# Kernel optimization log

Measured on AMD Instinct MI355X. Metric: run time of the kernel, lower is better.

The kernel has to match this reference:

```python
import jax, jax.numpy as jnp
import numpy as np

B, S, E, H = 4, 2048, 1024, 16
D = E // H  # head_dim


def setup_inputs() -> dict:
    key = jax.random.key(0)
    ks = jax.random.split(key, 7)
    scale = 1.0 / np.sqrt(E)
    return {
        "query": jax.random.normal(ks[0], (B, S, E), dtype=jnp.float32),
        "key": jax.random.normal(ks[1], (B, S, E), dtype=jnp.float32),
        "value": jax.random.normal(ks[2], (B, S, E), dtype=jnp.float32),
        "Wq": jax.random.normal(ks[3], (E, E), dtype=jnp.float32) * scale,
        "Wk": jax.random.normal(ks[4], (E, E), dtype=jnp.float32) * scale,
        "Wv": jax.random.normal(ks[5], (E, E), dtype=jnp.float32) * scale,
        "Wo": jax.random.normal(ks[6], (E, E), dtype=jnp.float32) * scale,
    }


def reference(query, key, value, Wq, Wk, Wv, Wo):
    b, s, e = query.shape
    sm_scale = (e // H) ** -0.5
    # TTLinear: x @ W.T; reshape to [b, h, s, d]
    q = (query @ Wq.T).reshape(b, s, H, D).transpose(0, 2, 1, 3)
    k = (key @ Wk.T).reshape(b, s, H, D).transpose(0, 2, 1, 3)
    v = (value @ Wv.T).reshape(b, s, H, D).transpose(0, 2, 1, 3)
    scores = jnp.einsum("bhqd,bhkd->bhqk", q, k) * sm_scale  # [b,h,s,s]
    attn = jax.nn.softmax(scores, axis=-1)
    out = jnp.einsum("bhqk,bhkd->bhqd", attn, v)
    out = out.transpose(0, 2, 1, 3).reshape(b, s, e)
    # dropout is identity in eval mode
    return out @ Wo.T
```

## Files before the change

### kernel.cpp

```cpp
#include <hip/hip_runtime.h>
#include <hip/hip_bf16.h>

#define BB 4
#define SS 2048
#define EE 1024
#define HH 16
#define DD 64
#define MM (BB*SS)

using f16x8 = __attribute__((ext_vector_type(8))) _Float16;
using f16x4 = __attribute__((ext_vector_type(4))) _Float16;
using f32x4 = __attribute__((ext_vector_type(4))) float;
using f32x16 = __attribute__((ext_vector_type(16))) float;

typedef __attribute__((address_space(3))) void       as3_void;
typedef const __attribute__((address_space(1))) void as1_cvoid;

__device__ __forceinline__ void async16(void* lds, const void* g) {
    __builtin_amdgcn_global_load_lds((as1_cvoid*)g, (as3_void*)lds, 16, 0, 0);
}

__device__ __forceinline__ f16x8 cvt8(const float* src) {
    const float4 v0 = *(const float4*)src;
    const float4 v1 = *(const float4*)(src + 4);
    f16x8 h;
    h[0] = (_Float16)v0.x; h[1] = (_Float16)v0.y;
    h[2] = (_Float16)v0.z; h[3] = (_Float16)v0.w;
    h[4] = (_Float16)v1.x; h[5] = (_Float16)v1.y;
    h[6] = (_Float16)v1.z; h[7] = (_Float16)v1.w;
    return h;
}

__global__ __launch_bounds__(256) void cvt_all(const float* __restrict__ q,
                                               const float* __restrict__ k,
                                               const float* __restrict__ v,
                                               const float* __restrict__ w0,
                                               const float* __restrict__ w1,
                                               const float* __restrict__ w2,
                                               const float* __restrict__ w3,
                                               _Float16* __restrict__ dq,
                                               _Float16* __restrict__ dk,
                                               _Float16* __restrict__ dv,
                                               _Float16* __restrict__ wf,
                                               int aN8, int wN8) {
    int seg = blockIdx.y;
    int i = blockIdx.x * 256 + threadIdx.x;
    const float* s; _Float16* d; int n8;
    if (seg < 3) {
        s = seg == 0 ? q : seg == 1 ? k : v;
        d = seg == 0 ? dq : seg == 1 ? dk : dv;
        n8 = aN8;
    } else {
        int t = seg - 3;
        s = t == 0 ? w0 : t == 1 ? w1 : t == 2 ? w2 : w3;
        d = wf + (size_t)t * EE * EE;
        n8 = wN8;
    }
    if (i < n8) ((f16x8*)d)[i] = cvt8(s + (size_t)i * 8);
}

__device__ __forceinline__ void swizzle512(int fid, int& m0, int& n0) {
    int xcd  = fid & 7;
    int s    = fid >> 3;
    int band = xcd + 8 * (s >> 5);
    int w    = s & 31;
    m0 = (band * 4 + (w & 3)) * 128;
    n0 = (w >> 2) * 128;
}

__global__ __launch_bounds__(256) void gemm_qkv(const _Float16* __restrict__ A0,
                                                const _Float16* __restrict__ A1,
                                                const _Float16* __restrict__ A2,
                                                const _Float16* __restrict__ W,
                                                _Float16* __restrict__ Cb,
                                                int M, int N, int K) {
    constexpr int BM = 128, BN = 128, BK = 64;
    __shared__ alignas(16) _Float16 As[2][BM * 32];
    __shared__ alignas(16) _Float16 Bs[2][BN * 32];

    const int tid  = threadIdx.x;
    const int lane = tid & 63;
    const int wave = tid >> 6;
    const int wm   = (wave >> 1) * 64;
    const int wn   = (wave & 1) * 64;
    const int quad = lane >> 4;
    const int c    = lane & 15;
    int m0, n0;
    swizzle512(blockIdx.x, m0, n0);
    const int z = blockIdx.y;

    const _Float16* A  = z == 0 ? A0 : z == 1 ? A1 : A2;
    const _Float16* Bw = W + (size_t)z * EE * EE;
    _Float16* C = Cb + (size_t)z * MM * EE;
    const float osc = (z == 0) ? 0.18033688f : 1.0f;

    f32x4 acc[4][4] = {};

    for (int k0 = 0; k0 < K; k0 += BK) {
#pragma unroll
        for (int p = 0; p < 4; ++p) {
            int half = p >> 1;
            int remb = (p & 1) * 256 + wave * 64;
            int rem  = remb + lane;
            int row  = rem >> 2, kc = (rem & 3) * 8;
            async16(&As[half][remb * 8], A  + (size_t)(m0 + row) * K + k0 + half * 32 + kc);
            async16(&Bs[half][remb * 8], Bw + (size_t)(n0 + row) * K + k0 + half * 32 + kc);
        }
        __syncthreads();

#pragma unroll
        for (int ks = 0; ks < 2; ++ks) {
            f16x8 af[4], bf[4];
#pragma unroll
            for (int i = 0; i < 4; ++i)
                af[i] = *(const f16x8*)&As[ks][(wm + i * 16 + c) * 32 + quad * 8];
#pragma unroll
            for (int j = 0; j < 4; ++j)
                bf[j] = *(const f16x8*)&Bs[ks][(wn + j * 16 + c) * 32 + quad * 8];
#pragma unroll
            for (int i = 0; i < 4; ++i)
#pragma unroll
                for (int j = 0; j < 4; ++j)
                    acc[i][j] = __builtin_amdgcn_mfma_f32_16x16x32_f16(af[i], bf[j], acc[i][j], 0, 0, 0);
        }
        __syncthreads();
    }

    if (z == 2) {
        _Float16* tb = (wave < 2) ? ((_Float16*)As) + wave * 4096
                                  : ((_Float16*)Bs) + (wave - 2) * 4096;
#pragma unroll
        for (int i = 0; i < 4; ++i)
#pragma unroll
            for (int j = 0; j < 4; ++j) {
                int dl = j * 16 + c;
                int sl = i * 16 + quad * 4;
                f16x4 ov;
#pragma unroll
                for (int r = 0; r < 4; ++r) ov[r] = (_Float16)acc[i][j][r];
                *(f16x4*)&tb[dl * 64 + (sl ^ ((dl & 7) << 3))] = ov;
            }
        __syncthreads();
        const int colbase = n0 + wn;
        const int h  = colbase >> 6;
        const int rowb = m0 + wm;
        const int bq = rowb >> 11;
        const int s_base = rowb & 2047;
        const int dr0 = lane >> 3;
        const int sc  = (lane & 7) * 8;
        _Float16* Vtb = C + (((size_t)bq * HH + h) * DD) * SS;
#pragma unroll
        for (int dd = 0; dd < 8; ++dd) {
            int d = dd * 8 + dr0;
            f16x8 vv = *(const f16x8*)&tb[d * 64 + (sc ^ ((d & 7) << 3))];
            *(f16x8*)&Vtb[(size_t)d * SS + s_base + sc] = vv;
        }
    } else {
#pragma unroll
        for (int i = 0; i < 4; ++i)
#pragma unroll
            for (int j = 0; j < 4; ++j)
#pragma unroll
                for (int r = 0; r < 4; ++r) {
                    int row = m0 + wm + i * 16 + quad * 4 + r;
                    int col = n0 + wn + j * 16 + c;
                    C[(size_t)row * N + col] = (_Float16)(acc[i][j][r] * osc);
                }
    }
}

__global__ __launch_bounds__(256) void gemm_wo(const _Float16* __restrict__ A,
                                               const _Float16* __restrict__ Bw,
                                               float* __restrict__ C,
                                               int M, int N, int K) {
    constexpr int BM = 128, BN = 128, BK = 64;
    __shared__ alignas(16) _Float16 As[2][BM * 32];
    __shared__ alignas(16) _Float16 Bs[2][BN * 32];

    const int tid  = threadIdx.x;
    const int lane = tid & 63;
    const int wave = tid >> 6;
    const int wm   = (wave >> 1) * 64;
    const int wn   = (wave & 1) * 64;
    const int quad = lane >> 4;
    const int c    = lane & 15;
    int m0, n0;
    swizzle512(blockIdx.x, m0, n0);

    f32x4 acc[4][4] = {};

    for (int k0 = 0; k0 < K; k0 += BK) {
#pragma unroll
        for (int p = 0; p < 4; ++p) {
            int half = p >> 1;
            int remb = (p & 1) * 256 + wave * 64;
            int rem  = remb + lane;
            int row  = rem >> 2, kc = (rem & 3) * 8;
            async16(&As[half][remb * 8], A  + (size_t)(m0 + row) * K + k0 + half * 32 + kc);
            async16(&Bs[half][remb * 8], Bw + (size_t)(n0 + row) * K + k0 + half * 32 + kc);
        }
        __syncthreads();

#pragma unroll
        for (int ks = 0; ks < 2; ++ks) {
            f16x8 af[4], bf[4];
#pragma unroll
            for (int i = 0; i < 4; ++i)
                af[i] = *(const f16x8*)&As[ks][(wm + i * 16 + c) * 32 + quad * 8];
#pragma unroll
            for (int j = 0; j < 4; ++j)
                bf[j] = *(const f16x8*)&Bs[ks][(wn + j * 16 + c) * 32 + quad * 8];
#pragma unroll
            for (int i = 0; i < 4; ++i)
#pragma unroll
                for (int j = 0; j < 4; ++j)
                    acc[i][j] = __builtin_amdgcn_mfma_f32_16x16x32_f16(af[i], bf[j], acc[i][j], 0, 0, 0);
        }
        __syncthreads();
    }

#pragma unroll
    for (int i = 0; i < 4; ++i)
#pragma unroll
        for (int j = 0; j < 4; ++j)
#pragma unroll
            for (int r = 0; r < 4; ++r) {
                int row = m0 + wm + i * 16 + quad * 4 + r;
                int col = n0 + wn + j * 16 + c;
                C[(size_t)row * N + col] = acc[i][j][r];
            }
}

__global__ __launch_bounds__(256, 4) void attn_kernel(const _Float16* __restrict__ Q,
                                                      const _Float16* __restrict__ K,
                                                      const _Float16* __restrict__ Vt,
                                                      _Float16* __restrict__ O) {
    constexpr int NT = SS / 64;
    __shared__ alignas(16) _Float16 Ks[2][8 * 512];
    __shared__ alignas(16) _Float16 Vs[2][8 * 512];

    const int tid  = threadIdx.x;
    const int lane = tid & 63;
    const int wave = tid >> 6;
    const int l31  = lane & 31;
    const int hl   = lane >> 5;
    const int bh   = blockIdx.x;
    const int b    = bh >> 4, h = bh & 15;
    const int q0   = blockIdx.y * 128;

    const _Float16* Qg  = Q  + (size_t)(b * SS + q0) * EE + h * DD;
    const _Float16* Kg  = K  + (size_t)(b * SS) * EE + h * DD;
    const _Float16* Vtg = Vt + (size_t)bh * DD * SS;

    f16x8 qf[4];
#pragma unroll
    for (int ks = 0; ks < 4; ++ks)
        qf[ks] = *(const f16x8*)(Qg + (size_t)(wave * 32 + l31) * EE + ks * 16 + hl * 8);

    const _Float16* kp[2];
    const _Float16* vp[2];
#pragma unroll
    for (int p = 0; p < 2; ++p) {
        int f = wave * 2 + p;
        int kvt = f >> 2, ksk = f & 3;
        kp[p] = Kg + (size_t)(kvt * 32 + l31) * EE + ksk * 16 + hl * 8;
        int ksv = f >> 1, dt = f & 1;
        vp[p] = Vtg + (size_t)(dt * 32 + l31) * SS + ksv * 16 + hl * 8;
    }

#pragma unroll
    for (int p = 0; p < 2; ++p) {
        int f = wave * 2 + p;
        async16(&Ks[0][f * 512], kp[p]);
        async16(&Vs[0][f * 512], vp[p]);
    }
    __syncthreads();

    float ls[4] = {0.f, 0.f, 0.f, 0.f};
    f32x16 o0 = {}, o1 = {};

    for (int t = 0; t < NT; ++t) {
        const int buf = t & 1;

        if (t + 1 < NT) {
#pragma unroll
            for (int p = 0; p < 2; ++p) {
                int f = wave * 2 + p;
                kp[p] += 64 * EE;
                vp[p] += 64;
                async16(&Ks[buf ^ 1][f * 512], kp[p]);
                async16(&Vs[buf ^ 1][f * 512], vp[p]);
            }
        }

        f32x16 sa = {}, sb = {};
        __builtin_amdgcn_s_setprio(1);
#pragma unroll
        for (int ks = 0; ks < 4; ++ks) {
            f16x8 a0 = *(const f16x8*)&Ks[buf][ks * 512 + lane * 8];
            f16x8 a1 = *(const f16x8*)&Ks[buf][(4 + ks) * 512 + lane * 8];
            sa = __builtin_amdgcn_mfma_f32_32x32x16_f16(a0, qf[ks], sa, 0, 0, 0);
            sb = __builtin_amdgcn_mfma_f32_32x32x16_f16(a1, qf[ks], sb, 0, 0, 0);
        }
        __builtin_amdgcn_s_setprio(0);

        f16x8 pB[4];
#pragma unroll
        for (int kvt = 0; kvt < 2; ++kvt) {
            const f32x16& s = kvt ? sb : sa;
            float p[16];
#pragma unroll
            for (int r = 0; r < 16; ++r) {
                p[r] = __builtin_amdgcn_exp2f(s[r]);
                ls[r & 3] += p[r];
            }
            int w[8];
#pragma unroll
            for (int i = 0; i < 8; ++i)
                w[i] = __builtin_bit_cast(int, __builtin_amdgcn_cvt_pkrtz(p[2 * i], p[2 * i + 1]));
            asm("v_permlane32_swap_b32 %0, %1" : "+v"(w[0]), "+v"(w[2]));
            asm("v_permlane32_swap_b32 %0, %1" : "+v"(w[1]), "+v"(w[3]));
            asm("v_permlane32_swap_b32 %0, %1" : "+v"(w[4]), "+v"(w[6]));
            asm("v_permlane32_swap_b32 %0, %1" : "+v"(w[5]), "+v"(w[7]));
            int4 lo; lo.x = w[0]; lo.y = w[1]; lo.z = w[2]; lo.w = w[3];
            int4 hi; hi.x = w[4]; hi.y = w[5]; hi.z = w[6]; hi.w = w[7];
            pB[kvt * 2 + 0] = __builtin_bit_cast(f16x8, lo);
            pB[kvt * 2 + 1] = __builtin_bit_cast(f16x8, hi);

            __builtin_amdgcn_s_setprio(1);
#pragma unroll
            for (int ks = kvt * 2; ks < kvt * 2 + 2; ++ks) {
                f16x8 v0 = *(const f16x8*)&Vs[buf][(ks * 2 + 0) * 512 + lane * 8];
                o0 = __builtin_amdgcn_mfma_f32_32x32x16_f16(v0, pB[ks], o0, 0, 0, 0);
                f16x8 v1 = *(const f16x8*)&Vs[buf][(ks * 2 + 1) * 512 + lane * 8];
                o1 = __builtin_amdgcn_mfma_f32_32x32x16_f16(v1, pB[ks], o1, 0, 0, 0);
            }
            __builtin_amdgcn_s_setprio(0);
        }

        __syncthreads();
    }

    float lsum = (ls[0] + ls[1]) + (ls[2] + ls[3]);
    float lt  = lsum + __shfl_xor(lsum, 32);
    float inv = 1.0f / lt;
    _Float16* Og = O + (size_t)(b * SS + q0 + wave * 32 + l31) * EE + h * DD;
#pragma unroll
    for (int dt = 0; dt < 2; ++dt)
#pragma unroll
        for (int g = 0; g < 4; ++g) {
            f16x4 ov;
#pragma unroll
            for (int r = 0; r < 4; ++r) {
                float val = (dt == 0) ? o0[g * 4 + r] : o1[g * 4 + r];
                ov[r] = (_Float16)(val * inv);
            }
            *(f16x4*)&Og[dt * 32 + g * 8 + hl * 4] = ov;
        }
}

extern "C" void kernel_launch(void* const* d_in, const int* in_sizes, int n_in,
                              void* d_out, int out_size, void* d_ws, size_t ws_size,
                              hipStream_t stream) {
    const float* query = (const float*)d_in[0];
    const float* key   = (const float*)d_in[1];
    const float* value = (const float*)d_in[2];
    const float* Wq    = (const float*)d_in[3];
    const float* Wk    = (const float*)d_in[4];
    const float* Wv    = (const float*)d_in[5];
    const float* Wo    = (const float*)d_in[6];
    float* out = (float*)d_out;

    const size_t NE = (size_t)MM * EE;
    const size_t NW = (size_t)EE * EE;
    _Float16* Qw   = (_Float16*)d_ws;
    _Float16* Kw   = Qw + NE;
    _Float16* Vw   = Kw + NE;
    _Float16* Wf   = Vw + NE;
    _Float16* Qact = Wf + 4 * NW;
    _Float16* Kact = (_Float16*)d_out;
    _Float16* Vact = Kact + NE;

    dim3 blk(256);
    const int wN8 = (int)(NW / 8), aN8 = (int)(NE / 8);

    cvt_all<<<dim3(aN8 / 256, 7), blk, 0, stream>>>(query, key, value, Wq, Wk, Wv, Wo,
                                                    Qact, Kact, Vact, Wf, aN8, wN8);

    gemm_qkv<<<dim3(512, 3), blk, 0, stream>>>(Qact, Kact, Vact, Wf, Qw, MM, EE, EE);

    attn_kernel<<<dim3(BB * HH, SS / 128), blk, 0, stream>>>(Qw, Kw, Vw, Qact);

    gemm_wo<<<dim3(512), blk, 0, stream>>>(Qact, Wf + 3 * NW, out, MM, EE, EE);
}
```

Measured before the change: 337.6 us.

## Double-buffer LDS tiles in QKV and output-projection GEMMs to overlap loads with MFMA

```diff
diff --git a/kernel.cpp b/kernel.cpp
--- a/kernel.cpp
+++ b/kernel.cpp
@@ -75,8 +75,9 @@
                                                 _Float16* __restrict__ Cb,
                                                 int M, int N, int K) {
     constexpr int BM = 128, BN = 128, BK = 64;
-    __shared__ alignas(16) _Float16 As[2][BM * 32];
-    __shared__ alignas(16) _Float16 Bs[2][BN * 32];
+    constexpr int NSTEP = EE / BK;
+    __shared__ alignas(16) _Float16 As[2][2][BM * 32];
+    __shared__ alignas(16) _Float16 Bs[2][2][BN * 32];
 
     const int tid  = threadIdx.x;
     const int lane = tid & 63;
@@ -94,29 +95,38 @@
     _Float16* C = Cb + (size_t)z * MM * EE;
     const float osc = (z == 0) ? 0.18033688f : 1.0f;
 
+    const int remb0 = wave * 64;
+    const int remb1 = 256 + wave * 64;
     f32x4 acc[4][4] = {};
 
-    for (int k0 = 0; k0 < K; k0 += BK) {
+    auto STAGE = [&](int b, int k0) {
 #pragma unroll
         for (int p = 0; p < 4; ++p) {
             int half = p >> 1;
-            int remb = (p & 1) * 256 + wave * 64;
+            int remb = (p & 1) ? remb1 : remb0;
             int rem  = remb + lane;
             int row  = rem >> 2, kc = (rem & 3) * 8;
-            async16(&As[half][remb * 8], A  + (size_t)(m0 + row) * K + k0 + half * 32 + kc);
-            async16(&Bs[half][remb * 8], Bw + (size_t)(n0 + row) * K + k0 + half * 32 + kc);
-        }
-        __syncthreads();
+            async16(&As[b][half][remb * 8], A  + (size_t)(m0 + row) * K + k0 + half * 32 + kc);
+            async16(&Bs[b][half][remb * 8], Bw + (size_t)(n0 + row) * K + k0 + half * 32 + kc);
+        }
+    };
+
+    STAGE(0, 0);
+    __syncthreads();
+
+    for (int ki = 0; ki < NSTEP; ++ki) {
+        const int b = ki & 1;
+        if (ki + 1 < NSTEP) STAGE(b ^ 1, (ki + 1) * BK);
 
 #pragma unroll
         for (int ks = 0; ks < 2; ++ks) {
             f16x8 af[4], bf[4];
 #pragma unroll
             for (int i = 0; i < 4; ++i)
-                af[i] = *(const f16x8*)&As[ks][(wm + i * 16 + c) * 32 + quad * 8];
+                af[i] = *(const f16x8*)&As[b][ks][(wm + i * 16 + c) * 32 + quad * 8];
 #pragma unroll
             for (int j = 0; j < 4; ++j)
-                bf[j] = *(const f16x8*)&Bs[ks][(wn + j * 16 + c) * 32 + quad * 8];
+                bf[j] = *(const f16x8*)&Bs[b][ks][(wn + j * 16 + c) * 32 + quad * 8];
 #pragma unroll
             for (int i = 0; i < 4; ++i)
 #pragma unroll
@@ -127,8 +137,7 @@
     }
 
     if (z == 2) {
-        _Float16* tb = (wave < 2) ? ((_Float16*)As) + wave * 4096
-                                  : ((_Float16*)Bs) + (wave - 2) * 4096;
+        _Float16* tb = ((_Float16*)As) + wave * 4096;
 #pragma unroll
         for (int i = 0; i < 4; ++i)
 #pragma unroll
@@ -174,8 +183,9 @@
                                                float* __restrict__ C,
                                                int M, int N, int K) {
     constexpr int BM = 128, BN = 128, BK = 64;
-    __shared__ alignas(16) _Float16 As[2][BM * 32];
-    __shared__ alignas(16) _Float16 Bs[2][BN * 32];
+    constexpr int NSTEP = EE / BK;
+    __shared__ alignas(16) _Float16 As[2][2][BM * 32];
+    __shared__ alignas(16) _Float16 Bs[2][2][BN * 32];
 
     const int tid  = threadIdx.x;
     const int lane = tid & 63;
@@ -187,29 +197,38 @@
     int m0, n0;
     swizzle512(blockIdx.x, m0, n0);
 
+    const int remb0 = wave * 64;
+    const int remb1 = 256 + wave * 64;
     f32x4 acc[4][4] = {};
 
-    for (int k0 = 0; k0 < K; k0 += BK) {
+    auto STAGE = [&](int b, int k0) {
 #pragma unroll
         for (int p = 0; p < 4; ++p) {
             int half = p >> 1;
-            int remb = (p & 1) * 256 + wave * 64;
+            int remb = (p & 1) ? remb1 : remb0;
             int rem  = remb + lane;
             int row  = rem >> 2, kc = (rem & 3) * 8;
-            async16(&As[half][remb * 8], A  + (size_t)(m0 + row) * K + k0 + half * 32 + kc);
-            async16(&Bs[half][remb * 8], Bw + (size_t)(n0 + row) * K + k0 + half * 32 + kc);
-        }
-        __syncthreads();
+            async16(&As[b][half][remb * 8], A  + (size_t)(m0 + row) * K + k0 + half * 32 + kc);
+            async16(&Bs[b][half][remb * 8], Bw + (size_t)(n0 + row) * K + k0 + half * 32 + kc);
+        }
+    };
+
+    STAGE(0, 0);
+    __syncthreads();
+
+    for (int ki = 0; ki < NSTEP; ++ki) {
+        const int b = ki & 1;
+        if (ki + 1 < NSTEP) STAGE(b ^ 1, (ki + 1) * BK);
 
 #pragma unroll
         for (int ks = 0; ks < 2; ++ks) {
             f16x8 af[4], bf[4];
 #pragma unroll
             for (int i = 0; i < 4; ++i)
-                af[i] = *(const f16x8*)&As[ks][(wm + i * 16 + c) * 32 + quad * 8];
+                af[i] = *(const f16x8*)&As[b][ks][(wm + i * 16 + c) * 32 + quad * 8];
 #pragma unroll
             for (int j = 0; j < 4; ++j)
-                bf[j] = *(const f16x8*)&Bs[ks][(wn + j * 16 + c) * 32 + quad * 8];
+                bf[j] = *(const f16x8*)&Bs[b][ks][(wn + j * 16 + c) * 32 + quad * 8];
 #pragma unroll
             for (int i = 0; i < 4; ++i)
 #pragma unroll
```

Result: slower. 350.9 us (+3.9%).
